# Optimization experiments

Measured on AMD Instinct MI355X. Metric: run time of the kernel, lower is better.

The kernel has to match this reference:

```python
import jax, jax.numpy as jnp
import numpy as np

N_NODES = 100000
N_EDGES = 600000
DIM = 128
LN_EPS = 1e-5


def setup_inputs() -> dict:
    key = jax.random.key(0)
    ks = jax.random.split(key, 12)
    s = 1.0 / np.sqrt(DIM)
    return {
        "h": jax.random.normal(ks[0], (N_NODES, DIM), dtype=jnp.float32),
        "edge_src": jax.random.randint(ks[1], (N_EDGES,), 0, N_NODES, dtype=jnp.int32),
        "edge_dst": jax.random.randint(ks[2], (N_EDGES,), 0, N_NODES, dtype=jnp.int32),
        "W_self": jax.random.uniform(ks[3], (DIM, DIM), jnp.float32, -s, s),
        "b_self": jax.random.uniform(ks[4], (DIM,), jnp.float32, -s, s),
        "W_neigh": jax.random.uniform(ks[5], (DIM, DIM), jnp.float32, -s, s),
        "b_neigh": jax.random.uniform(ks[6], (DIM,), jnp.float32, -s, s),
        "W_gate": jax.random.uniform(ks[7], (DIM, 2 * DIM), jnp.float32, -s, s),
        "b_gate": jax.random.uniform(ks[8], (DIM,), jnp.float32, -s, s),
        "ln_gamma": jnp.ones((DIM,), jnp.float32),
        "ln_beta": jnp.zeros((DIM,), jnp.float32),
    }


def reference(h, edge_src, edge_dst, W_self, b_self, W_neigh, b_neigh, W_gate, b_gate, ln_gamma, ln_beta):
    n = h.shape[0]
    # self transform: [N, D]
    hs = h @ W_self.T + b_self
    # mean over predecessors via segment sum over edges (src -> dst)
    neigh_sum = jax.ops.segment_sum(h[edge_src], edge_dst, num_segments=n)
    counts = jax.ops.segment_sum(jnp.ones((edge_src.shape[0],), h.dtype), edge_dst, num_segments=n)
    has_pred = (counts > 0).astype(h.dtype)[:, None]
    neigh_mean = neigh_sum / jnp.maximum(counts, 1.0)[:, None]
    hn = neigh_mean @ W_neigh.T + b_neigh
    # nodes with no predecessors skip the neighbor term entirely (incl. bias)
    m = hs + has_pred * hn
    gate = jax.nn.sigmoid(jnp.concatenate([h, m], axis=-1) @ W_gate.T + b_gate)
    v = gate * m + (1.0 - gate) * h
    # LayerNorm (biased variance, as torch) + relu
    mu = jnp.mean(v, axis=-1, keepdims=True)
    var = jnp.mean(jnp.square(v - mu), axis=-1, keepdims=True)
    out = (v - mu) * jax.lax.rsqrt(var + LN_EPS) * ln_gamma + ln_beta
    return jax.nn.relu(out)
```

## Files before the change

kernel.cpp:

```cpp
#include <hip/hip_runtime.h>
#include <math.h>

#define N_NODES 100000
#define N_EDGES 600000
#define DIM 128
#define LN_EPS 1e-5f
#define SCAN_NBLK ((N_NODES + 255) / 256)
#define NTILES ((N_NODES + 127) / 128)
#define NODE_GRID 256

typedef __bf16 bf16x8 __attribute__((ext_vector_type(8)));
typedef __bf16 bf16x4 __attribute__((ext_vector_type(4)));
typedef float f32x4 __attribute__((ext_vector_type(4)));

__global__ __launch_bounds__(256)
void prep_kernel(const float* __restrict__ h, const int* __restrict__ edst,
                 __bf16* __restrict__ h_bf, int* __restrict__ counts) {
  int i = blockIdx.x * 256 + threadIdx.x;
  {
    const float4 v0 = *reinterpret_cast<const float4*>(h + (size_t)i * 8);
    const float4 v1 = *reinterpret_cast<const float4*>(h + (size_t)i * 8 + 4);
    bf16x8 b;
    b[0] = (__bf16)v0.x; b[1] = (__bf16)v0.y; b[2] = (__bf16)v0.z; b[3] = (__bf16)v0.w;
    b[4] = (__bf16)v1.x; b[5] = (__bf16)v1.y; b[6] = (__bf16)v1.z; b[7] = (__bf16)v1.w;
    *reinterpret_cast<bf16x8*>(h_bf + (size_t)i * 8) = b;
  }
  if (i < N_EDGES) atomicAdd(&counts[edst[i]], 1);
}

__global__ __launch_bounds__(256)
void scan1_kernel(const int* __restrict__ counts, int* __restrict__ block_sums) {
  int i = blockIdx.x * 256 + threadIdx.x;
  int v = (i < N_NODES) ? counts[i] : 0;
#pragma unroll
  for (int off = 1; off < 64; off <<= 1) v += __shfl_xor(v, off);
  __shared__ int ws[4];
  if ((threadIdx.x & 63) == 0) ws[threadIdx.x >> 6] = v;
  __syncthreads();
  if (threadIdx.x == 0) block_sums[blockIdx.x] = ws[0] + ws[1] + ws[2] + ws[3];
}

__global__ __launch_bounds__(512)
void scan2_kernel(int* __restrict__ block_sums) {
  __shared__ int sh[512];
  int t = threadIdx.x;
  int v = (t < SCAN_NBLK) ? block_sums[t] : 0;
  sh[t] = v;
  __syncthreads();
#pragma unroll
  for (int off = 1; off < 512; off <<= 1) {
    int u = (t >= off) ? sh[t - off] : 0;
    __syncthreads();
    sh[t] += u;
    __syncthreads();
  }
  if (t < SCAN_NBLK) block_sums[t] = (t == 0) ? 0 : sh[t - 1];
}

__global__ __launch_bounds__(256)
void scan3_kernel(const int* __restrict__ counts, const int* __restrict__ block_excl,
                  int* __restrict__ row_off, int* __restrict__ cursor) {
  int i = blockIdx.x * 256 + threadIdx.x;
  int t = threadIdx.x;
  int lane = t & 63, wv = t >> 6;
  int v = (i < N_NODES) ? counts[i] : 0;
  int s = v;
#pragma unroll
  for (int off = 1; off < 64; off <<= 1) {
    int u = __shfl_up(s, off);
    if (lane >= off) s += u;
  }
  __shared__ int wtot[4];
  if (lane == 63) wtot[wv] = s;
  __syncthreads();
  int wo = 0;
  for (int w = 0; w < wv; ++w) wo += wtot[w];
  int excl = block_excl[blockIdx.x] + wo + (s - v);
  if (i < N_NODES) { row_off[i] = excl; cursor[i] = 0; }
  if (i == 0) row_off[N_NODES] = N_EDGES;
}

__global__ void csr_fill_kernel(const int* __restrict__ esrc, const int* __restrict__ edst,
                                const int* __restrict__ row_off, int* __restrict__ cursor,
                                int* __restrict__ csr_src) {
  int e = blockIdx.x * 256 + threadIdx.x;
  if (e >= N_EDGES) return;
  int d = edst[e];
  int pos = atomicAdd(&cursor[d], 1);
  csr_src[row_off[d] + pos] = esrc[e];
}

__global__ __launch_bounds__(256)
void gather_kernel(const __bf16* __restrict__ h_bf, const int* __restrict__ csr_src,
                   const int* __restrict__ row_off, __bf16* __restrict__ mean_bf) {
  int node = blockIdx.x * 8 + (threadIdx.x >> 5);
  if (node >= N_NODES) return;
  int t = threadIdx.x & 31;
  int b = row_off[node], e = row_off[node + 1];
  float acc0 = 0.f, acc1 = 0.f, acc2 = 0.f, acc3 = 0.f;
  int i = b;
  for (; i + 4 <= e; i += 4) {
    int s0 = csr_src[i], s1 = csr_src[i + 1], s2 = csr_src[i + 2], s3 = csr_src[i + 3];
    bf16x4 v0 = *reinterpret_cast<const bf16x4*>(h_bf + (size_t)s0 * DIM + t * 4);
    bf16x4 v1 = *reinterpret_cast<const bf16x4*>(h_bf + (size_t)s1 * DIM + t * 4);
    bf16x4 v2 = *reinterpret_cast<const bf16x4*>(h_bf + (size_t)s2 * DIM + t * 4);
    bf16x4 v3 = *reinterpret_cast<const bf16x4*>(h_bf + (size_t)s3 * DIM + t * 4);
    acc0 += (float)v0[0] + (float)v1[0] + (float)v2[0] + (float)v3[0];
    acc1 += (float)v0[1] + (float)v1[1] + (float)v2[1] + (float)v3[1];
    acc2 += (float)v0[2] + (float)v1[2] + (float)v2[2] + (float)v3[2];
    acc3 += (float)v0[3] + (float)v1[3] + (float)v2[3] + (float)v3[3];
  }
  for (; i < e; ++i) {
    int s = csr_src[i];
    bf16x4 v = *reinterpret_cast<const bf16x4*>(h_bf + (size_t)s * DIM + t * 4);
    acc0 += (float)v[0]; acc1 += (float)v[1]; acc2 += (float)v[2]; acc3 += (float)v[3];
  }
  float inv = (e > b) ? 1.0f / (float)(e - b) : 0.0f;
  bf16x4 mv;
  mv[0] = (__bf16)(acc0 * inv); mv[1] = (__bf16)(acc1 * inv);
  mv[2] = (__bf16)(acc2 * inv); mv[3] = (__bf16)(acc3 * inv);
  *reinterpret_cast<bf16x4*>(mean_bf + (size_t)node * DIM + t * 4) = mv;
}

__global__ __launch_bounds__(512, 1)
void node_kernel(const __bf16* __restrict__ h_bf,
                 const __bf16* __restrict__ mean_bf,
                 const int* __restrict__ counts,
                 const float* __restrict__ Wself,
                 const float* __restrict__ Wneigh,
                 const float* __restrict__ Wgate,
                 const float* __restrict__ b_self,
                 const float* __restrict__ b_neigh,
                 const float* __restrict__ b_gate,
                 const float* __restrict__ ln_g,
                 const float* __restrict__ ln_b,
                 float* __restrict__ out) {
  __shared__ __align__(16) char smem[163840];
  char* Wl = smem;

  const int tid = threadIdx.x;

  for (int c = tid; c < 8192; c += 512) {
    int mi = c >> 11;
    int w = c & 2047;
    int row = w >> 4, col8 = w & 15;
    const float* src;
    if (mi == 0)      src = Wself  + row * 128 + col8 * 8;
    else if (mi == 1) src = Wneigh + row * 128 + col8 * 8;
    else if (mi == 2) src = Wgate  + row * 256 + col8 * 8;
    else              src = Wgate  + row * 256 + 128 + col8 * 8;
    float4 v0 = *reinterpret_cast<const float4*>(src);
    float4 v1 = *reinterpret_cast<const float4*>(src + 4);
    bf16x8 b;
    b[0] = (__bf16)v0.x; b[1] = (__bf16)v0.y; b[2] = (__bf16)v0.z; b[3] = (__bf16)v0.w;
    b[4] = (__bf16)v1.x; b[5] = (__bf16)v1.y; b[6] = (__bf16)v1.z; b[7] = (__bf16)v1.w;
    int byte = (row * 256 + col8 * 16) ^ ((row & 7) << 4);
    *reinterpret_cast<bf16x8*>(Wl + mi * 32768 + byte) = b;
  }
  __syncthreads();

  const int lane = tid & 63;
  const int wave = tid >> 6;
  const int col = lane & 15;
  const int kb = (lane >> 4) << 3;
  const int rloc = (lane >> 4) << 2;
  char* Ms = smem + 131072 + wave * 4096;

  for (int tile = blockIdx.x; tile < NTILES; tile += NODE_GRID) {
    const int node0 = tile * 128;

    bf16x8 a_h[4], a_m[4];
    {
      int n_a = node0 + wave * 16 + col;
      if (n_a < N_NODES) {
#pragma unroll
        for (int k0 = 0; k0 < 4; ++k0) {
          int koff = k0 * 32 + kb;
          a_h[k0] = *reinterpret_cast<const bf16x8*>(h_bf + (size_t)n_a * DIM + koff);
          a_m[k0] = *reinterpret_cast<const bf16x8*>(mean_bf + (size_t)n_a * DIM + koff);
        }
      } else {
#pragma unroll
        for (int k0 = 0; k0 < 4; ++k0)
#pragma unroll
          for (int j = 0; j < 8; ++j) { a_h[k0][j] = (__bf16)0.f; a_m[k0][j] = (__bf16)0.f; }
      }
    }

    int4 c4 = *reinterpret_cast<const int4*>(counts + node0 + wave * 16 + rloc);
    float hp[4];
    {
      int nb0 = node0 + wave * 16 + rloc;
      hp[0] = (nb0 + 0 < N_NODES && c4.x > 0) ? 1.f : 0.f;
      hp[1] = (nb0 + 1 < N_NODES && c4.y > 0) ? 1.f : 0.f;
      hp[2] = (nb0 + 2 < N_NODES && c4.z > 0) ? 1.f : 0.f;
      hp[3] = (nb0 + 3 < N_NODES && c4.w > 0) ? 1.f : 0.f;
    }

    f32x4 sacc[8], nacc[8];
#pragma unroll
    for (int i = 0; i < 8; ++i) {
      sacc[i] = (f32x4){0.f, 0.f, 0.f, 0.f};
      nacc[i] = (f32x4){0.f, 0.f, 0.f, 0.f};
    }
#pragma unroll
    for (int k0 = 0; k0 < 4; ++k0) {
      int koff2 = (k0 * 32 + kb) * 2;
#pragma unroll
      for (int nb = 0; nb < 8; ++nb) {
        int row = nb * 16 + col;
        int swz = (row * 256 + koff2) ^ ((row & 7) << 4);
        bf16x8 bs = *reinterpret_cast<const bf16x8*>(Wl + swz);
        bf16x8 bn = *reinterpret_cast<const bf16x8*>(Wl + 32768 + swz);
        sacc[nb] = __builtin_amdgcn_mfma_f32_16x16x32_bf16(a_h[k0], bs, sacc[nb], 0, 0, 0);
        nacc[nb] = __builtin_amdgcn_mfma_f32_16x16x32_bf16(a_m[k0], bn, nacc[nb], 0, 0, 0);
      }
    }

#pragma unroll
    for (int nb = 0; nb < 8; ++nb) {
      int d = nb * 16 + col;
      float bs = b_self[d], bn = b_neigh[d];
#pragma unroll
      for (int r = 0; r < 4; ++r) {
        float mval = sacc[nb][r] + bs + hp[r] * (nacc[nb][r] + bn);
        sacc[nb][r] = mval;
        int rl = rloc + r;
        int byte = (rl * 256 + d * 2) ^ ((rl & 7) << 4);
        *reinterpret_cast<__bf16*>(Ms + byte) = (__bf16)mval;
      }
    }

    f32x4 gacc[8];
#pragma unroll
    for (int i = 0; i < 8; ++i) gacc[i] = (f32x4){0.f, 0.f, 0.f, 0.f};
#pragma unroll
    for (int k0 = 0; k0 < 4; ++k0) {
      int koff2 = (k0 * 32 + kb) * 2;
      int abyte = (col * 256 + koff2) ^ ((col & 7) << 4);
      bf16x8 am2 = *reinterpret_cast<const bf16x8*>(Ms + abyte);
#pragma unroll
      for (int nb = 0; nb < 8; ++nb) {
        int row = nb * 16 + col;
        int swz = (row * 256 + koff2) ^ ((row & 7) << 4);
        bf16x8 bgh = *reinterpret_cast<const bf16x8*>(Wl + 65536 + swz);
        bf16x8 bgm = *reinterpret_cast<const bf16x8*>(Wl + 98304 + swz);
        gacc[nb] = __builtin_amdgcn_mfma_f32_16x16x32_bf16(a_h[k0], bgh, gacc[nb], 0, 0, 0);
        gacc[nb] = __builtin_amdgcn_mfma_f32_16x16x32_bf16(am2, bgm, gacc[nb], 0, 0, 0);
      }
    }

#pragma unroll
    for (int k0 = 0; k0 < 4; ++k0) {
      int byte = (col * 256 + (k0 * 32 + kb) * 2) ^ ((col & 7) << 4);
      *reinterpret_cast<bf16x8*>(Ms + byte) = a_h[k0];
    }

    float s1[4] = {0.f, 0.f, 0.f, 0.f}, s2[4] = {0.f, 0.f, 0.f, 0.f};
#pragma unroll
    for (int nb = 0; nb < 8; ++nb) {
      int d = nb * 16 + col;
      float bg = b_gate[d];
#pragma unroll
      for (int r = 0; r < 4; ++r) {
        int rl = rloc + r;
        int byte = (rl * 256 + d * 2) ^ ((rl & 7) << 4);
        float hval = (float)*reinterpret_cast<const __bf16*>(Ms + byte);
        float g = 1.0f / (1.0f + __expf(-(gacc[nb][r] + bg)));
        float v = g * sacc[nb][r] + (1.0f - g) * hval;
        s1[r] += v;
        s2[r] += v * v;
        *reinterpret_cast<__bf16*>(Ms + byte) = (__bf16)v;
      }
    }
#pragma unroll
    for (int off = 1; off < 16; off <<= 1) {
#pragma unroll
      for (int r = 0; r < 4; ++r) {
        s1[r] += __shfl_xor(s1[r], off);
        s2[r] += __shfl_xor(s2[r], off);
      }
    }
    float mu[4], rs[4];
#pragma unroll
    for (int r = 0; r < 4; ++r) {
      mu[r] = s1[r] * (1.0f / DIM);
      float var = s2[r] * (1.0f / DIM) - mu[r] * mu[r];
      rs[r] = rsqrtf(var + LN_EPS);
    }

    {
      int orow = lane >> 2;
      int ochunk = lane & 3;
      int gn = node0 + wave * 16 + orow;
      int rsel = orow & 3;
      float muv = (rsel & 2) ? ((rsel & 1) ? mu[3] : mu[2]) : ((rsel & 1) ? mu[1] : mu[0]);
      float rsv = (rsel & 2) ? ((rsel & 1) ? rs[3] : rs[2]) : ((rsel & 1) ? rs[1] : rs[0]);
      bool valid = gn < N_NODES;
#pragma unroll
      for (int j = 0; j < 4; ++j) {
        int d0 = ochunk * 8 + j * 32;
        int byte = (orow * 256 + d0 * 2) ^ ((orow & 7) << 4);
        bf16x8 vb = *reinterpret_cast<const bf16x8*>(Ms + byte);
        float4 g0 = *reinterpret_cast<const float4*>(ln_g + d0);
        float4 g1 = *reinterpret_cast<const float4*>(ln_g + d0 + 4);
        float4 e0 = *reinterpret_cast<const float4*>(ln_b + d0);
        float4 e1 = *reinterpret_cast<const float4*>(ln_b + d0 + 4);
        float4 o0, o1;
        o0.x = fmaxf(((float)vb[0] - muv) * rsv * g0.x + e0.x, 0.f);
        o0.y = fmaxf(((float)vb[1] - muv) * rsv * g0.y + e0.y, 0.f);
        o0.z = fmaxf(((float)vb[2] - muv) * rsv * g0.z + e0.z, 0.f);
        o0.w = fmaxf(((float)vb[3] - muv) * rsv * g0.w + e0.w, 0.f);
        o1.x = fmaxf(((float)vb[4] - muv) * rsv * g1.x + e1.x, 0.f);
        o1.y = fmaxf(((float)vb[5] - muv) * rsv * g1.y + e1.y, 0.f);
        o1.z = fmaxf(((float)vb[6] - muv) * rsv * g1.z + e1.z, 0.f);
        o1.w = fmaxf(((float)vb[7] - muv) * rsv * g1.w + e1.w, 0.f);
        if (valid) {
          *reinterpret_cast<float4*>(out + (size_t)gn * DIM + d0) = o0;
          *reinterpret_cast<float4*>(out + (size_t)gn * DIM + d0 + 4) = o1;
        }
      }
    }
  }
}

extern "C" void kernel_launch(void* const* d_in, const int* in_sizes, int n_in,
                              void* d_out, int out_size, void* d_ws, size_t ws_size,
                              hipStream_t stream) {
  const float* h      = (const float*)d_in[0];
  const int*   esrc   = (const int*)d_in[1];
  const int*   edst   = (const int*)d_in[2];
  const float* Wself  = (const float*)d_in[3];
  const float* bself  = (const float*)d_in[4];
  const float* Wneigh = (const float*)d_in[5];
  const float* bneigh = (const float*)d_in[6];
  const float* Wgate  = (const float*)d_in[7];
  const float* bgate  = (const float*)d_in[8];
  const float* ln_g   = (const float*)d_in[9];
  const float* ln_b   = (const float*)d_in[10];
  float* out = (float*)d_out;

  char* ws = (char*)d_ws;
  int* counts   = (int*)ws;
  int* row_off  = (int*)(ws + 400384);
  int* cursor   = (int*)(ws + 800768);
  int* csr_src  = (int*)(ws + 1200768);
  int* blk_sums = (int*)(ws + 3600768);
  __bf16* h_bf    = (__bf16*)(ws + 3602432);
  __bf16* mean_bf = (__bf16*)(ws + 29202432);

  hipMemsetAsync(counts, 0, (size_t)N_NODES * sizeof(int), stream);

  prep_kernel<<<6250, 256, 0, stream>>>(h, edst, h_bf, counts);
  scan1_kernel<<<SCAN_NBLK, 256, 0, stream>>>(counts, blk_sums);
  scan2_kernel<<<1, 512, 0, stream>>>(blk_sums);
  scan3_kernel<<<SCAN_NBLK, 256, 0, stream>>>(counts, blk_sums, row_off, cursor);
  csr_fill_kernel<<<(N_EDGES + 255) / 256, 256, 0, stream>>>(esrc, edst, row_off, cursor, csr_src);
  gather_kernel<<<(N_NODES + 7) / 8, 256, 0, stream>>>(h_bf, csr_src, row_off, mean_bf);
  node_kernel<<<NODE_GRID, 512, 0, stream>>>(
      h_bf, mean_bf, counts, Wself, Wneigh, Wgate,
      bself, bneigh, bgate, ln_g, ln_b, out);
}
```

Baseline: 157.5 us.

## Fuse scan passes, vectorize CSR fill, widen gather loads to 16 bytes

Drops the single-block scan2 kernel: each scan3 block now sums the preceding block totals itself, which saves one launch at the cost of redundant reads of block_sums. The CSR fill handles four edges per thread using int4 loads. The gather uses 16 lanes per node with 8-element bf16 loads and batches of 8 neighbor indices to raise memory-level parallelism. The cost is a few masked loads on the last partial batch of each node.

```diff
diff --git a/kernel.cpp b/kernel.cpp
--- a/kernel.cpp
+++ b/kernel.cpp
@@ -40,29 +40,23 @@
   if (threadIdx.x == 0) block_sums[blockIdx.x] = ws[0] + ws[1] + ws[2] + ws[3];
 }
 
-__global__ __launch_bounds__(512)
-void scan2_kernel(int* __restrict__ block_sums) {
-  __shared__ int sh[512];
-  int t = threadIdx.x;
-  int v = (t < SCAN_NBLK) ? block_sums[t] : 0;
-  sh[t] = v;
+__global__ __launch_bounds__(256)
+void scan3_kernel(const int* __restrict__ counts, const int* __restrict__ block_sums,
+                  int* __restrict__ row_off, int* __restrict__ cursor) {
+  const int i = blockIdx.x * 256 + threadIdx.x;
+  const int t = threadIdx.x;
+  const int lane = t & 63, wv = t >> 6;
+  __shared__ int wtot[4];
+  __shared__ int sbase[4];
+
+  int partial = 0;
+  for (int j = t; j < blockIdx.x; j += 256) partial += block_sums[j];
+#pragma unroll
+  for (int off = 1; off < 64; off <<= 1) partial += __shfl_xor(partial, off);
+  if (lane == 0) sbase[wv] = partial;
   __syncthreads();
-#pragma unroll
-  for (int off = 1; off < 512; off <<= 1) {
-    int u = (t >= off) ? sh[t - off] : 0;
-    __syncthreads();
-    sh[t] += u;
-    __syncthreads();
-  }
-  if (t < SCAN_NBLK) block_sums[t] = (t == 0) ? 0 : sh[t - 1];
-}
-
-__global__ __launch_bounds__(256)
-void scan3_kernel(const int* __restrict__ counts, const int* __restrict__ block_excl,
-                  int* __restrict__ row_off, int* __restrict__ cursor) {
-  int i = blockIdx.x * 256 + threadIdx.x;
-  int t = threadIdx.x;
-  int lane = t & 63, wv = t >> 6;
+  const int base = sbase[0] + sbase[1] + sbase[2] + sbase[3];
+
   int v = (i < N_NODES) ? counts[i] : 0;
   int s = v;
 #pragma unroll
@@ -70,56 +64,74 @@
     int u = __shfl_up(s, off);
     if (lane >= off) s += u;
   }
-  __shared__ int wtot[4];
   if (lane == 63) wtot[wv] = s;
   __syncthreads();
   int wo = 0;
   for (int w = 0; w < wv; ++w) wo += wtot[w];
-  int excl = block_excl[blockIdx.x] + wo + (s - v);
+  int excl = base + wo + (s - v);
   if (i < N_NODES) { row_off[i] = excl; cursor[i] = 0; }
   if (i == 0) row_off[N_NODES] = N_EDGES;
 }
 
-__global__ void csr_fill_kernel(const int* __restrict__ esrc, const int* __restrict__ edst,
-                                const int* __restrict__ row_off, int* __restrict__ cursor,
-                                int* __restrict__ csr_src) {
-  int e = blockIdx.x * 256 + threadIdx.x;
-  if (e >= N_EDGES) return;
-  int d = edst[e];
-  int pos = atomicAdd(&cursor[d], 1);
-  csr_src[row_off[d] + pos] = esrc[e];
+__global__ __launch_bounds__(256)
+void csr_fill_kernel(const int* __restrict__ esrc, const int* __restrict__ edst,
+                     const int* __restrict__ row_off, int* __restrict__ cursor,
+                     int* __restrict__ csr_src) {
+  int base = (blockIdx.x * 256 + threadIdx.x) * 4;
+  if (base >= N_EDGES) return;
+  int4 s4 = *reinterpret_cast<const int4*>(esrc + base);
+  int4 d4 = *reinterpret_cast<const int4*>(edst + base);
+  {
+    int pos = atomicAdd(&cursor[d4.x], 1);
+    csr_src[row_off[d4.x] + pos] = s4.x;
+  }
+  {
+    int pos = atomicAdd(&cursor[d4.y], 1);
+    csr_src[row_off[d4.y] + pos] = s4.y;
+  }
+  {
+    int pos = atomicAdd(&cursor[d4.z], 1);
+    csr_src[row_off[d4.z] + pos] = s4.z;
+  }
+  {
+    int pos = atomicAdd(&cursor[d4.w], 1);
+    csr_src[row_off[d4.w] + pos] = s4.w;
+  }
 }
 
 __global__ __launch_bounds__(256)
 void gather_kernel(const __bf16* __restrict__ h_bf, const int* __restrict__ csr_src,
                    const int* __restrict__ row_off, __bf16* __restrict__ mean_bf) {
-  int node = blockIdx.x * 8 + (threadIdx.x >> 5);
+  int node = blockIdx.x * 16 + (threadIdx.x >> 4);
   if (node >= N_NODES) return;
-  int t = threadIdx.x & 31;
+  int t = threadIdx.x & 15;
   int b = row_off[node], e = row_off[node + 1];
-  float acc0 = 0.f, acc1 = 0.f, acc2 = 0.f, acc3 = 0.f;
-  int i = b;
-  for (; i + 4 <= e; i += 4) {
-    int s0 = csr_src[i], s1 = csr_src[i + 1], s2 = csr_src[i + 2], s3 = csr_src[i + 3];
-    bf16x4 v0 = *reinterpret_cast<const bf16x4*>(h_bf + (size_t)s0 * DIM + t * 4);
-    bf16x4 v1 = *reinterpret_cast<const bf16x4*>(h_bf + (size_t)s1 * DIM + t * 4);
-    bf16x4 v2 = *reinterpret_cast<const bf16x4*>(h_bf + (size_t)s2 * DIM + t * 4);
-    bf16x4 v3 = *reinterpret_cast<const bf16x4*>(h_bf + (size_t)s3 * DIM + t * 4);
-    acc0 += (float)v0[0] + (float)v1[0] + (float)v2[0] + (float)v3[0];
-    acc1 += (float)v0[1] + (float)v1[1] + (float)v2[1] + (float)v3[1];
-    acc2 += (float)v0[2] + (float)v1[2] + (float)v2[2] + (float)v3[2];
-    acc3 += (float)v0[3] + (float)v1[3] + (float)v2[3] + (float)v3[3];
-  }
-  for (; i < e; ++i) {
-    int s = csr_src[i];
-    bf16x4 v = *reinterpret_cast<const bf16x4*>(h_bf + (size_t)s * DIM + t * 4);
-    acc0 += (float)v[0]; acc1 += (float)v[1]; acc2 += (float)v[2]; acc3 += (float)v[3];
+  float acc[8];
+#pragma unroll
+  for (int j = 0; j < 8; ++j) acc[j] = 0.f;
+  for (int i = b; i < e; i += 8) {
+    int idx[8];
+#pragma unroll
+    for (int j = 0; j < 8; ++j) idx[j] = (i + j < e) ? csr_src[i + j] : -1;
+    bf16x8 v[8];
+#pragma unroll
+    for (int j = 0; j < 8; ++j) {
+      if (idx[j] >= 0)
+        v[j] = *reinterpret_cast<const bf16x8*>(h_bf + (size_t)idx[j] * DIM + t * 8);
+      else
+#pragma unroll
+        for (int k = 0; k < 8; ++k) v[j][k] = (__bf16)0.f;
+    }
+#pragma unroll
+    for (int j = 0; j < 8; ++j)
+#pragma unroll
+      for (int k = 0; k < 8; ++k) acc[k] += (float)v[j][k];
   }
   float inv = (e > b) ? 1.0f / (float)(e - b) : 0.0f;
-  bf16x4 mv;
-  mv[0] = (__bf16)(acc0 * inv); mv[1] = (__bf16)(acc1 * inv);
-  mv[2] = (__bf16)(acc2 * inv); mv[3] = (__bf16)(acc3 * inv);
-  *reinterpret_cast<bf16x4*>(mean_bf + (size_t)node * DIM + t * 4) = mv;
+  bf16x8 mv;
+#pragma unroll
+  for (int j = 0; j < 8; ++j) mv[j] = (__bf16)(acc[j] * inv);
+  *reinterpret_cast<bf16x8*>(mean_bf + (size_t)node * DIM + t * 8) = mv;
 }
 
 __global__ __launch_bounds__(512, 1)
@@ -353,10 +365,9 @@
 
   prep_kernel<<<6250, 256, 0, stream>>>(h, edst, h_bf, counts);
   scan1_kernel<<<SCAN_NBLK, 256, 0, stream>>>(counts, blk_sums);
-  scan2_kernel<<<1, 512, 0, stream>>>(blk_sums);
   scan3_kernel<<<SCAN_NBLK, 256, 0, stream>>>(counts, blk_sums, row_off, cursor);
-  csr_fill_kernel<<<(N_EDGES + 255) / 256, 256, 0, stream>>>(esrc, edst, row_off, cursor, csr_src);
-  gather_kernel<<<(N_NODES + 7) / 8, 256, 0, stream>>>(h_bf, csr_src, row_off, mean_bf);
+  csr_fill_kernel<<<(N_EDGES / 4 + 255) / 256, 256, 0, stream>>>(esrc, edst, row_off, cursor, csr_src);
+  gather_kernel<<<(N_NODES + 15) / 16, 256, 0, stream>>>(h_bf, csr_src, row_off, mean_bf);
   node_kernel<<<NODE_GRID, 512, 0, stream>>>(
       h_bf, mean_bf, counts, Wself, Wneigh, Wgate,
       bself, bneigh, bgate, ln_g, ln_b, out);
```

After: 154.3 us. -2.0%, faster.
